# Kernel tuning notes

Hardware: AMD Instinct MI355X
Metric: run time of the kernel (lower is better)

The kernel has to match this reference:

```python
import jax, jax.numpy as jnp
import numpy as np

N_NODES = 100000
LN_EPS = 1e-5
NEG_SLOPE = 0.2


def setup_inputs() -> dict:
    key = jax.random.key(0)
    ks = jax.random.split(key, 6)
    N, E, NIN, EDIM, NOUT, H = N_NODES, 1600000, 64, 32, 128, 4
    x = jax.random.normal(ks[0], (N, NIN), dtype=jnp.float32)
    edge_index = jax.random.randint(ks[1], (2, E), 0, N, dtype=jnp.int64)
    edge_attr = jax.random.normal(ks[2], (E, EDIM), dtype=jnp.float32)
    # xavier-uniform linear weights (torch layout: [out, in])
    def xavier(k, fan_out, fan_in):
        lim = float(np.sqrt(6.0 / (fan_in + fan_out)))
        return jax.random.uniform(k, (fan_out, fan_in), jnp.float32, -lim, lim)
    W_msg = xavier(ks[3], NOUT, NIN + EDIM)          # (128, 96)
    W_att = xavier(ks[4], H, 2 * NIN + EDIM)         # (4, 160)
    bias = jnp.zeros((NOUT,), jnp.float32)
    ln_gamma = jnp.ones((NOUT,), jnp.float32)
    ln_beta = jnp.zeros((NOUT,), jnp.float32)
    return {"x": x, "edge_index": edge_index, "edge_attr": edge_attr,
            "W_msg": W_msg, "W_att": W_att, "bias": bias,
            "ln_gamma": ln_gamma, "ln_beta": ln_beta}


def reference(x, edge_index, edge_attr, W_msg, W_att, bias, ln_gamma, ln_beta):
    N = x.shape[0]
    H = W_att.shape[0]
    src, dst = edge_index[0], edge_index[1]
    xs = x[src]                                       # (E, node_in) gather
    xd = x[dst]                                       # (E, node_in) gather
    # message: W_msg @ [h_u ; x_uv]
    msg_in = jnp.concatenate([xs, edge_attr], axis=-1)            # (E, 96)
    msgs = msg_in @ W_msg.T                                        # (E, out_dim)
    msgs = msgs.reshape(-1, H, W_msg.shape[0] // H)                # (E, H, D)
    # attention logits: LeakyReLU(W_att @ [h_u ; h_v ; x_uv])
    att_in = jnp.concatenate([xs, xd, edge_attr], axis=-1)         # (E, 160)
    logits = att_in @ W_att.T                                      # (E, H)
    logits = jax.nn.leaky_relu(logits, NEG_SLOPE)
    # per-destination-node sparse softmax
    seg_max = jax.ops.segment_max(logits, dst, num_segments=N)     # (N, H)
    exp_l = jnp.exp(logits - seg_max[dst])                         # (E, H)
    seg_sum = jax.ops.segment_sum(exp_l, dst, num_segments=N)      # (N, H)
    att = exp_l / (seg_sum[dst] + 1e-9)                            # (E, H)
    # weighted scatter-add aggregation
    weighted = msgs * att[..., None]                               # (E, H, D)
    out = jax.ops.segment_sum(weighted, dst, num_segments=N)       # (N, H, D)
    out = out.reshape(N, -1) + bias                                # concat heads
    # layer norm over feature dim
    mu = out.mean(axis=-1, keepdims=True)
    var = out.var(axis=-1, keepdims=True)
    out = (out - mu) * jax.lax.rsqrt(var + LN_EPS) * ln_gamma + ln_beta
    return out
```

## Files before the change

### kernel.cpp

```cpp
#include <hip/hip_runtime.h>
#include <hip/hip_bf16.h>

typedef __attribute__((ext_vector_type(8))) short short8;
typedef __attribute__((ext_vector_type(4))) float f32x4;

__device__ __forceinline__ unsigned short fbf(float f) {
  union { float f; unsigned u; } v; v.f = f;
  unsigned r = v.u + 0x7fffu + ((v.u >> 16) & 1u);
  return (unsigned short)(r >> 16);
}
__device__ __forceinline__ unsigned pk2(float a, float b) {
  return (unsigned)fbf(a) | ((unsigned)fbf(b) << 16);
}
__device__ __forceinline__ float ubf(unsigned hi) {
  union { unsigned u; float f; } v; v.u = hi << 16; return v.f;
}
__device__ __forceinline__ float dot4(float4 a, float4 b) {
  return fmaf(a.x, b.x, fmaf(a.y, b.y, fmaf(a.z, b.z, a.w * b.w)));
}

__global__ void k_count(const int* __restrict__ dst, int E, int* __restrict__ deg) {
  for (int i = blockIdx.x * blockDim.x + threadIdx.x; i < E; i += gridDim.x * blockDim.x)
    atomicAdd(&deg[dst[i]], 1);
}

__global__ void k_scan1(const int* __restrict__ deg, int N, int* __restrict__ part,
                        int* __restrict__ bsum) {
  __shared__ int tmp[1024];
  int tid = threadIdx.x;
  int i = blockIdx.x * 1024 + tid;
  int v = (i < N) ? deg[i] : 0;
  tmp[tid] = v;
  __syncthreads();
  for (int ofs = 1; ofs < 1024; ofs <<= 1) {
    int t = (tid >= ofs) ? tmp[tid - ofs] : 0;
    __syncthreads();
    tmp[tid] += t;
    __syncthreads();
  }
  if (i < N) part[i] = tmp[tid] - v;
  if (tid == 1023) bsum[blockIdx.x] = tmp[tid];
}

__global__ void k_scan2(int* __restrict__ part, const int* __restrict__ bsum, int N,
                        int* __restrict__ cursor) {
  __shared__ int sbase;
  if (threadIdx.x == 0) {
    int b = 0;
    for (int j = 0; j < (int)blockIdx.x; j++) b += bsum[j];
    sbase = b;
  }
  __syncthreads();
  int i = blockIdx.x * 1024 + threadIdx.x;
  if (i < N) {
    int o = part[i] + sbase;
    part[i] = o;
    cursor[i] = o;
  }
}

__global__ void k_fill(const int* __restrict__ src, const int* __restrict__ dst, int E,
                       int* __restrict__ cursor, int2* __restrict__ csr2) {
  for (int i = blockIdx.x * blockDim.x + threadIdx.x; i < E; i += gridDim.x * blockDim.x) {
    int d = dst[i];
    int slot = atomicAdd(&cursor[d], 1);
    csr2[slot] = make_int2(src[i], i);
  }
}

__launch_bounds__(256)
__global__ void k_prep(const float* __restrict__ x, const float* __restrict__ W_att,
                       float4* __restrict__ A_s, float4* __restrict__ A_d,
                       unsigned* __restrict__ xb32, int N) {
  __shared__ float4 s_wa[160];
  if (threadIdx.x < 160) s_wa[threadIdx.x] = ((const float4*)W_att)[threadIdx.x];
  __syncthreads();
  for (int v = blockIdx.x * blockDim.x + threadIdx.x; v < N; v += gridDim.x * blockDim.x) {
    const float4* xp = (const float4*)&x[v * 64];
    float4 xq[16];
    #pragma unroll
    for (int k = 0; k < 16; k++) xq[k] = xp[k];
    float as[4] = {}, ad[4] = {};
    #pragma unroll
    for (int h = 0; h < 4; h++) {
      #pragma unroll
      for (int k = 0; k < 16; k++) {
        as[h] += dot4(s_wa[h * 40 + k], xq[k]);
        ad[h] += dot4(s_wa[h * 40 + 16 + k], xq[k]);
      }
    }
    A_s[v] = make_float4(as[0], as[1], as[2], as[3]);
    A_d[v] = make_float4(ad[0], ad[1], ad[2], ad[3]);
    #pragma unroll
    for (int k = 0; k < 16; k++) {
      xb32[v * 32 + 2 * k]     = pk2(xq[k].x, xq[k].y);
      xb32[v * 32 + 2 * k + 1] = pk2(xq[k].z, xq[k].w);
    }
  }
}

__launch_bounds__(256)
__global__ void k_agg(const unsigned short* __restrict__ xb, const float* __restrict__ ea,
                      const float4* __restrict__ A_s, const float4* __restrict__ A_d,
                      const int2* __restrict__ csr2, const int* __restrict__ offsets,
                      const int* __restrict__ deg, const float* __restrict__ W_att,
                      unsigned short* __restrict__ agg, float* __restrict__ denom, int N) {
  __shared__ int2 s_ids[4][32];
  __shared__ float4 s_att[4][8];
  const int lane = threadIdx.x & 63;
  const int wvb = threadIdx.x >> 6;
  const int wv = (blockIdx.x * blockDim.x + threadIdx.x) >> 6;
  const int nw = (gridDim.x * blockDim.x) >> 6;
  const int l32 = lane & 31;
  const bool hi = (lane & 32) != 0;
  const int pj = lane >> 3;
  const int jc = lane & 7;
  const float jc0f = (jc == 0) ? 1.f : 0.f;

  const float4 wea0 = *(const float4*)&W_att[0 * 160 + 128 + jc * 4];
  const float4 wea1 = *(const float4*)&W_att[1 * 160 + 128 + jc * 4];
  const float4 wea2 = *(const float4*)&W_att[2 * 160 + 128 + jc * 4];
  const float4 wea3 = *(const float4*)&W_att[3 * 160 + 128 + jc * 4];

  unsigned short axv[8], bxv[8];
  float aev[8], bev[8];
  float4 aef, aasv, bef, basv;

#define REFILL(g) do {                                                      \
    if (((g) & 3) == 0) {                                                   \
      int2 q_ = csr2[start + min((g) * 8 + l32, dg - 1)];                   \
      if (lane < 32) s_ids[wvb][l32] = q_;                                  \
    }                                                                       \
  } while (0)

#define ISSUE_G(X, E4, AS, g) do {                                          \
    const int qo_ = ((g) & 3) * 8;                                          \
    _Pragma("unroll")                                                       \
    for (int p = 0; p < 8; p++) {                                           \
      int2 t_ = s_ids[wvb][qo_ + p];                                        \
      X[p] = xb[(size_t)t_.x * 64 + lane];                                  \
      E4[p] = ea[(size_t)t_.y * 32 + l32];                                  \
    }                                                                       \
    int2 idl_ = s_ids[wvb][qo_ + pj];                                       \
    AS##ef = *(const float4*)&ea[(size_t)idl_.y * 32 + jc * 4];             \
    AS##asv = A_s[idl_.x];                                                  \
  } while (0)

#define COMPUTE_G(X, E4, AS, g) do {                                        \
    float lp0 = dot4(wea0, AS##ef), lp1 = dot4(wea1, AS##ef);               \
    float lp2 = dot4(wea2, AS##ef), lp3 = dot4(wea3, AS##ef);               \
    _Pragma("unroll")                                                       \
    for (int m = 1; m <= 4; m <<= 1) {                                      \
      lp0 += __shfl_xor(lp0, m, 64); lp1 += __shfl_xor(lp1, m, 64);         \
      lp2 += __shfl_xor(lp2, m, 64); lp3 += __shfl_xor(lp3, m, 64);         \
    }                                                                       \
    const float msk_ = ((g) * 8 + pj < dg) ? 1.f : 0.f;                     \
    float4 av_; float lg_;                                                  \
    lg_ = lp0 + AS##asv.x + adv.x; lg_ = (lg_ > 0.f) ? lg_ : 0.2f * lg_;    \
    av_.x = msk_ * __expf(lg_);                                             \
    lg_ = lp1 + AS##asv.y + adv.y; lg_ = (lg_ > 0.f) ? lg_ : 0.2f * lg_;    \
    av_.y = msk_ * __expf(lg_);                                             \
    lg_ = lp2 + AS##asv.z + adv.z; lg_ = (lg_ > 0.f) ? lg_ : 0.2f * lg_;    \
    av_.z = msk_ * __expf(lg_);                                             \
    lg_ = lp3 + AS##asv.w + adv.w; lg_ = (lg_ > 0.f) ? lg_ : 0.2f * lg_;    \
    av_.w = msk_ * __expf(lg_);                                             \
    if (jc == 0) s_att[wvb][pj] = av_;                                      \
    ssa.x = fmaf(av_.x, jc0f, ssa.x); ssa.y = fmaf(av_.y, jc0f, ssa.y);     \
    ssa.z = fmaf(av_.z, jc0f, ssa.z); ssa.w = fmaf(av_.w, jc0f, ssa.w);     \
    _Pragma("unroll")                                                       \
    for (int p = 0; p < 8; p++) {                                           \
      float4 ap = s_att[wvb][p];                                            \
      float xf = ubf((unsigned)X[p]);                                       \
      ax0 = fmaf(ap.x, xf, ax0); ax1 = fmaf(ap.y, xf, ax1);                 \
      ax2 = fmaf(ap.z, xf, ax2); ax3 = fmaf(ap.w, xf, ax3);                 \
      ae0 = fmaf(hi ? ap.z : ap.x, E4[p], ae0);                             \
      ae1 = fmaf(hi ? ap.w : ap.y, E4[p], ae1);                             \
    }                                                                       \
  } while (0)

  int v = wv;
  int start = 0, dg = 0;
  float4 adv = make_float4(0.f, 0.f, 0.f, 0.f);
  if (v < N) { start = offsets[v]; dg = deg[v]; adv = A_d[v]; }

  while (v < N) {
    const int v_next = v + nw;
    const int vc = min(v_next, N - 1);
    const int start_n = offsets[vc];
    const int dg_n = deg[vc];
    const float4 adv_n = A_d[vc];

    float ax0 = 0, ax1 = 0, ax2 = 0, ax3 = 0, ae0 = 0, ae1 = 0;
    float4 ssa = make_float4(0.f, 0.f, 0.f, 0.f);

    if (dg > 0) {
      const int ng = (dg + 7) >> 3;
      {
        int2 q_ = csr2[start + min(l32, dg - 1)];
        if (lane < 32) s_ids[wvb][l32] = q_;
      }
      ISSUE_G(axv, aev, a, 0);
      int g = 0;
      while (true) {
        if (g + 1 < ng) { REFILL(g + 1); ISSUE_G(bxv, bev, b, g + 1); }
        COMPUTE_G(axv, aev, a, g);
        if (++g >= ng) break;
        if (g + 1 < ng) { REFILL(g + 1); ISSUE_G(axv, aev, a, g + 1); }
        COMPUTE_G(bxv, bev, b, g);
        if (++g >= ng) break;
      }
    }

    #pragma unroll
    for (int m = 1; m <= 32; m <<= 1) {
      ssa.x += __shfl_xor(ssa.x, m, 64);
      ssa.y += __shfl_xor(ssa.y, m, 64);
      ssa.z += __shfl_xor(ssa.z, m, 64);
      ssa.w += __shfl_xor(ssa.w, m, 64);
    }
    const int base = v * 384;
    agg[base + lane]       = fbf(ax0);
    agg[base + 96 + lane]  = fbf(ax1);
    agg[base + 192 + lane] = fbf(ax2);
    agg[base + 288 + lane] = fbf(ax3);
    const int hA = hi ? 2 : 0;
    agg[base + hA * 96 + 64 + l32]       = fbf(ae0);
    agg[base + (hA + 1) * 96 + 64 + l32] = fbf(ae1);
    if (lane == 0) ((float4*)denom)[v] = ssa;

    v = v_next; start = start_n; dg = dg_n; adv = adv_n;
  }
#undef REFILL
#undef ISSUE_G
#undef COMPUTE_G
}

__launch_bounds__(128)
__global__ void k_out(const unsigned short* __restrict__ agg, const float* __restrict__ W_msg,
                      const float* __restrict__ denom, const float* __restrict__ bias,
                      const float* __restrict__ gamma, const float* __restrict__ beta,
                      float* __restrict__ out, int N, int T) {
  __shared__ float s_den[64];
  __shared__ float s_sum[2][16], s_sq[2][16];
  const int f = threadIdx.x;
  const int w = f >> 6;
  const int l = f & 63;
  const int c16 = l & 15;
  const int rg = l >> 4;

  short8 wb[2][2][3];
  float biasv[2][2], gv[2][2], bv[2][2];
  #pragma unroll
  for (int hh = 0; hh < 2; hh++) {
    const int head = 2 * w + hh;
    #pragma unroll
    for (int ct = 0; ct < 2; ct++) {
      const int q = head * 32 + ct * 16 + c16;
      biasv[hh][ct] = bias[q]; gv[hh][ct] = gamma[q]; bv[hh][ct] = beta[q];
      #pragma unroll
      for (int kk = 0; kk < 3; kk++) {
        const float* p = &W_msg[q * 96 + kk * 32 + rg * 8];
        short8 s;
        #pragma unroll
        for (int i = 0; i < 8; i++) s[i] = (short)fbf(p[i]);
        wb[hh][ct][kk] = s;
      }
    }
  }

  for (int t = blockIdx.x; t < T; t += gridDim.x) {
    const int n0 = t * 16;
    if (f < 64) s_den[f] = denom[min(n0 + (f >> 2), N - 1) * 4 + (f & 3)];
    __syncthreads();

    f32x4 c[2][2] = {{{0.f,0.f,0.f,0.f},{0.f,0.f,0.f,0.f}},
                     {{0.f,0.f,0.f,0.f},{0.f,0.f,0.f,0.f}}};
    const int nA = min(n0 + c16, N - 1);
    #pragma unroll
    for (int hh = 0; hh < 2; hh++) {
      const int head = 2 * w + hh;
      #pragma unroll
      for (int kk = 0; kk < 3; kk++) {
        short8 a = *(const short8*)&agg[nA * 384 + head * 96 + kk * 32 + rg * 8];
        c[hh][0] = __builtin_amdgcn_mfma_f32_16x16x32_bf16(a, wb[hh][0][kk], c[hh][0], 0, 0, 0);
        c[hh][1] = __builtin_amdgcn_mfma_f32_16x16x32_bf16(a, wb[hh][1][kk], c[hh][1], 0, 0, 0);
      }
    }

    float val[2][2][4];
    #pragma unroll
    for (int hh = 0; hh < 2; hh++)
      #pragma unroll
      for (int ct = 0; ct < 2; ct++)
        #pragma unroll
        for (int r = 0; r < 4; r++) {
          const float d = s_den[(rg * 4 + r) * 4 + (2 * w + hh)] + 1e-9f;
          val[hh][ct][r] = c[hh][ct][r] / d + biasv[hh][ct];
        }

    float sr[4], qr[4];
    #pragma unroll
    for (int r = 0; r < 4; r++) {
      float s = 0.f, q2 = 0.f;
      #pragma unroll
      for (int hh = 0; hh < 2; hh++)
        #pragma unroll
        for (int ct = 0; ct < 2; ct++) { s += val[hh][ct][r]; q2 = fmaf(val[hh][ct][r], val[hh][ct][r], q2); }
      #pragma unroll
      for (int m = 1; m <= 8; m <<= 1) { s += __shfl_xor(s, m, 64); q2 += __shfl_xor(q2, m, 64); }
      sr[r] = s; qr[r] = q2;
    }
    if (c16 == 0) {
      #pragma unroll
      for (int r = 0; r < 4; r++) { s_sum[w][rg * 4 + r] = sr[r]; s_sq[w][rg * 4 + r] = qr[r]; }
    }
    __syncthreads();

    float mean[4], rstd[4];
    #pragma unroll
    for (int r = 0; r < 4; r++) {
      const int ni = rg * 4 + r;
      mean[r] = (s_sum[0][ni] + s_sum[1][ni]) * (1.f / 128.f);
      const float m2 = (s_sq[0][ni] + s_sq[1][ni]) * (1.f / 128.f);
      rstd[r] = rsqrtf(m2 - mean[r] * mean[r] + 1e-5f);
    }
    #pragma unroll
    for (int hh = 0; hh < 2; hh++)
      #pragma unroll
      for (int ct = 0; ct < 2; ct++)
        #pragma unroll
        for (int r = 0; r < 4; r++) {
          const int n = n0 + rg * 4 + r;
          if (n < N)
            out[n * 128 + (2 * w + hh) * 32 + ct * 16 + c16] =
                (val[hh][ct][r] - mean[r]) * rstd[r] * gv[hh][ct] + bv[hh][ct];
        }
    __syncthreads();
  }
}

extern "C" void kernel_launch(void* const* d_in, const int* in_sizes, int n_in,
                              void* d_out, int out_size, void* d_ws, size_t ws_size,
                              hipStream_t stream) {
  const float* x     = (const float*)d_in[0];
  const int*   ei    = (const int*)d_in[1];
  const float* ea    = (const float*)d_in[2];
  const float* W_msg = (const float*)d_in[3];
  const float* W_att = (const float*)d_in[4];
  const float* bias  = (const float*)d_in[5];
  const float* gamma = (const float*)d_in[6];
  const float* beta  = (const float*)d_in[7];
  float* out = (float*)d_out;

  const int N = in_sizes[0] / 64;
  const int E = in_sizes[1] / 2;
  const int* esrc = ei;
  const int* edst = ei + E;

  char* p = (char*)d_ws;
  int* deg      = (int*)p;            p += (size_t)N * 4;
  int* offsets  = (int*)p;            p += (size_t)N * 4;
  int* cursor   = (int*)p;            p += (size_t)N * 4;
  int* bsum     = (int*)p;            p += 2048 * 4;
  int2* csr2    = (int2*)p;           p += (size_t)E * 8;
  float4* A_s   = (float4*)p;         p += (size_t)N * 16;
  float4* A_d   = (float4*)p;         p += (size_t)N * 16;
  unsigned short* xb = (unsigned short*)p; p += (size_t)N * 64 * 2;
  unsigned short* agg = (unsigned short*)p; p += (size_t)N * 384 * 2;
  float* denom  = (float*)p;

  hipMemsetAsync(deg, 0, (size_t)N * sizeof(int), stream);
  const int SB = (N + 1023) / 1024;
  const int T = (N + 15) / 16;

  k_count<<<2048, 256, 0, stream>>>(edst, E, deg);
  k_scan1<<<SB, 1024, 0, stream>>>(deg, N, offsets, bsum);
  k_scan2<<<SB, 1024, 0, stream>>>(offsets, bsum, N, cursor);
  k_fill<<<2048, 256, 0, stream>>>(esrc, edst, E, cursor, csr2);
  k_prep<<<(N + 255) / 256, 256, 0, stream>>>(x, W_att, A_s, A_d, (unsigned*)xb, N);
  k_agg<<<2048, 256, 0, stream>>>(xb, ea, A_s, A_d, csr2, offsets, deg, W_att,
                                  agg, denom, N);
  k_out<<<2048, 128, 0, stream>>>(agg, W_msg, denom, bias, gamma, beta, out, N, T);
}
```

Measured before the change: 418.7 us.

## Pipeline edge gathers across node boundaries in single-wave aggregation blocks

Restructures the aggregation kernel to one wave per block (8192 blocks of 64 threads) and makes the software pipeline continuous across nodes. The next node's CSR ids are prefetched and the first group of the next node is issued while the current node's last group computes, using double-buffered shared id slots. Edge-attribute loads are halved by having each half-wave load alternate edges and combine through a cross-half shuffle. This is meant to hide gather latency at node boundaries, which is costly with an average degree of about 16, in exchange for more register pressure and more complex control flow.

After: 425.7 us. Within noise of the previous version (+1.7%).

```diff
diff --git a/kernel.cpp b/kernel.cpp
--- a/kernel.cpp
+++ b/kernel.cpp
@@ -99,20 +99,20 @@
   }
 }
 
-__launch_bounds__(256)
+__launch_bounds__(64)
 __global__ void k_agg(const unsigned short* __restrict__ xb, const float* __restrict__ ea,
                       const float4* __restrict__ A_s, const float4* __restrict__ A_d,
                       const int2* __restrict__ csr2, const int* __restrict__ offsets,
                       const int* __restrict__ deg, const float* __restrict__ W_att,
-                      unsigned short* __restrict__ agg, float* __restrict__ denom, int N) {
-  __shared__ int2 s_ids[4][32];
-  __shared__ float4 s_att[4][8];
-  const int lane = threadIdx.x & 63;
-  const int wvb = threadIdx.x >> 6;
-  const int wv = (blockIdx.x * blockDim.x + threadIdx.x) >> 6;
-  const int nw = (gridDim.x * blockDim.x) >> 6;
+                      unsigned short* __restrict__ agg, float* __restrict__ denom,
+                      int N, int Ec) {
+  __shared__ int2 s_ids[2][32];
+  __shared__ float4 s_att[8];
+  const int lane = threadIdx.x;
+  const int nw = gridDim.x;
   const int l32 = lane & 31;
-  const bool hi = (lane & 32) != 0;
+  const bool hi = lane >= 32;
+  const int hsel = hi ? 1 : 0;
   const int pj = lane >> 3;
   const int jc = lane & 7;
   const float jc0f = (jc == 0) ? 1.f : 0.f;
@@ -123,32 +123,28 @@
   const float4 wea3 = *(const float4*)&W_att[3 * 160 + 128 + jc * 4];
 
   unsigned short axv[8], bxv[8];
-  float aev[8], bev[8];
+  float aev[4], bev[4];
   float4 aef, aasv, bef, basv;
 
-#define REFILL(g) do {                                                      \
-    if (((g) & 3) == 0) {                                                   \
-      int2 q_ = csr2[start + min((g) * 8 + l32, dg - 1)];                   \
-      if (lane < 32) s_ids[wvb][l32] = q_;                                  \
-    }                                                                       \
+#define ISSUE_G(X, E4, PF, sl, qo) do {                                     \
+    _Pragma("unroll")                                                       \
+    for (int p = 0; p < 8; p++) {                                           \
+      int2 t_ = s_ids[sl][(qo) + p];                                        \
+      X[p] = xb[(size_t)t_.x * 64 + lane];                                  \
+    }                                                                       \
+    _Pragma("unroll")                                                       \
+    for (int i = 0; i < 4; i++) {                                           \
+      int2 te_ = s_ids[sl][(qo) + 2 * i + hsel];                            \
+      E4[i] = ea[(size_t)te_.y * 32 + l32];                                 \
+    }                                                                       \
+    int2 idl_ = s_ids[sl][(qo) + pj];                                       \
+    PF##ef = *(const float4*)&ea[(size_t)idl_.y * 32 + jc * 4];             \
+    PF##asv = A_s[idl_.x];                                                  \
   } while (0)
 
-#define ISSUE_G(X, E4, AS, g) do {                                          \
-    const int qo_ = ((g) & 3) * 8;                                          \
-    _Pragma("unroll")                                                       \
-    for (int p = 0; p < 8; p++) {                                           \
-      int2 t_ = s_ids[wvb][qo_ + p];                                        \
-      X[p] = xb[(size_t)t_.x * 64 + lane];                                  \
-      E4[p] = ea[(size_t)t_.y * 32 + l32];                                  \
-    }                                                                       \
-    int2 idl_ = s_ids[wvb][qo_ + pj];                                       \
-    AS##ef = *(const float4*)&ea[(size_t)idl_.y * 32 + jc * 4];             \
-    AS##asv = A_s[idl_.x];                                                  \
-  } while (0)
-
-#define COMPUTE_G(X, E4, AS, g) do {                                        \
-    float lp0 = dot4(wea0, AS##ef), lp1 = dot4(wea1, AS##ef);               \
-    float lp2 = dot4(wea2, AS##ef), lp3 = dot4(wea3, AS##ef);               \
+#define COMPUTE_G(X, E4, PF, g) do {                                        \
+    float lp0 = dot4(wea0, PF##ef), lp1 = dot4(wea1, PF##ef);               \
+    float lp2 = dot4(wea2, PF##ef), lp3 = dot4(wea3, PF##ef);               \
     _Pragma("unroll")                                                       \
     for (int m = 1; m <= 4; m <<= 1) {                                      \
       lp0 += __shfl_xor(lp0, m, 64); lp1 += __shfl_xor(lp1, m, 64);         \
@@ -156,83 +152,118 @@
     }                                                                       \
     const float msk_ = ((g) * 8 + pj < dg) ? 1.f : 0.f;                     \
     float4 av_; float lg_;                                                  \
-    lg_ = lp0 + AS##asv.x + adv.x; lg_ = (lg_ > 0.f) ? lg_ : 0.2f * lg_;    \
+    lg_ = lp0 + PF##asv.x + adv.x; lg_ = (lg_ > 0.f) ? lg_ : 0.2f * lg_;    \
     av_.x = msk_ * __expf(lg_);                                             \
-    lg_ = lp1 + AS##asv.y + adv.y; lg_ = (lg_ > 0.f) ? lg_ : 0.2f * lg_;    \
+    lg_ = lp1 + PF##asv.y + adv.y; lg_ = (lg_ > 0.f) ? lg_ : 0.2f * lg_;    \
     av_.y = msk_ * __expf(lg_);                                             \
-    lg_ = lp2 + AS##asv.z + adv.z; lg_ = (lg_ > 0.f) ? lg_ : 0.2f * lg_;    \
+    lg_ = lp2 + PF##asv.z + adv.z; lg_ = (lg_ > 0.f) ? lg_ : 0.2f * lg_;    \
     av_.z = msk_ * __expf(lg_);                                             \
-    lg_ = lp3 + AS##asv.w + adv.w; lg_ = (lg_ > 0.f) ? lg_ : 0.2f * lg_;    \
+    lg_ = lp3 + PF##asv.w + adv.w; lg_ = (lg_ > 0.f) ? lg_ : 0.2f * lg_;    \
     av_.w = msk_ * __expf(lg_);                                             \
-    if (jc == 0) s_att[wvb][pj] = av_;                                      \
+    if (jc == 0) s_att[pj] = av_;                                           \
     ssa.x = fmaf(av_.x, jc0f, ssa.x); ssa.y = fmaf(av_.y, jc0f, ssa.y);     \
     ssa.z = fmaf(av_.z, jc0f, ssa.z); ssa.w = fmaf(av_.w, jc0f, ssa.w);     \
     _Pragma("unroll")                                                       \
     for (int p = 0; p < 8; p++) {                                           \
-      float4 ap = s_att[wvb][p];                                            \
+      float4 ap = s_att[p];                                                 \
       float xf = ubf((unsigned)X[p]);                                       \
       ax0 = fmaf(ap.x, xf, ax0); ax1 = fmaf(ap.y, xf, ax1);                 \
       ax2 = fmaf(ap.z, xf, ax2); ax3 = fmaf(ap.w, xf, ax3);                 \
-      ae0 = fmaf(hi ? ap.z : ap.x, E4[p], ae0);                             \
-      ae1 = fmaf(hi ? ap.w : ap.y, E4[p], ae1);                             \
+    }                                                                       \
+    _Pragma("unroll")                                                       \
+    for (int i = 0; i < 4; i++) {                                           \
+      float4 ap = s_att[2 * i + hsel];                                      \
+      ae0 = fmaf(ap.x, E4[i], ae0); ae1 = fmaf(ap.y, E4[i], ae1);           \
+      ae2 = fmaf(ap.z, E4[i], ae2); ae3 = fmaf(ap.w, E4[i], ae3);           \
     }                                                                       \
   } while (0)
 
-  int v = wv;
-  int start = 0, dg = 0;
-  float4 adv = make_float4(0.f, 0.f, 0.f, 0.f);
-  if (v < N) { start = offsets[v]; dg = deg[v]; adv = A_d[v]; }
-
-  while (v < N) {
-    const int v_next = v + nw;
-    const int vc = min(v_next, N - 1);
-    const int start_n = offsets[vc];
-    const int dg_n = deg[vc];
-    const float4 adv_n = A_d[vc];
-
-    float ax0 = 0, ax1 = 0, ax2 = 0, ax3 = 0, ae0 = 0, ae1 = 0;
-    float4 ssa = make_float4(0.f, 0.f, 0.f, 0.f);
-
-    if (dg > 0) {
-      const int ng = (dg + 7) >> 3;
-      {
-        int2 q_ = csr2[start + min(l32, dg - 1)];
-        if (lane < 32) s_ids[wvb][l32] = q_;
-      }
-      ISSUE_G(axv, aev, a, 0);
-      int g = 0;
-      while (true) {
-        if (g + 1 < ng) { REFILL(g + 1); ISSUE_G(bxv, bev, b, g + 1); }
-        COMPUTE_G(axv, aev, a, g);
-        if (++g >= ng) break;
-        if (g + 1 < ng) { REFILL(g + 1); ISSUE_G(axv, aev, a, g + 1); }
-        COMPUTE_G(bxv, bev, b, g);
-        if (++g >= ng) break;
-      }
-    }
-
-    #pragma unroll
-    for (int m = 1; m <= 32; m <<= 1) {
-      ssa.x += __shfl_xor(ssa.x, m, 64);
-      ssa.y += __shfl_xor(ssa.y, m, 64);
-      ssa.z += __shfl_xor(ssa.z, m, 64);
-      ssa.w += __shfl_xor(ssa.w, m, 64);
-    }
-    const int base = v * 384;
-    agg[base + lane]       = fbf(ax0);
-    agg[base + 96 + lane]  = fbf(ax1);
-    agg[base + 192 + lane] = fbf(ax2);
-    agg[base + 288 + lane] = fbf(ax3);
-    const int hA = hi ? 2 : 0;
-    agg[base + hA * 96 + 64 + l32]       = fbf(ae0);
-    agg[base + (hA + 1) * 96 + 64 + l32] = fbf(ae1);
-    if (lane == 0) ((float4*)denom)[v] = ssa;
-
-    v = v_next; start = start_n; dg = dg_n; adv = adv_n;
-  }
-#undef REFILL
+#define EPILOGUE_G do {                                                     \
+    ae0 += __shfl_xor(ae0, 32, 64); ae1 += __shfl_xor(ae1, 32, 64);         \
+    ae2 += __shfl_xor(ae2, 32, 64); ae3 += __shfl_xor(ae3, 32, 64);         \
+    _Pragma("unroll")                                                       \
+    for (int m = 1; m <= 32; m <<= 1) {                                     \
+      ssa.x += __shfl_xor(ssa.x, m, 64); ssa.y += __shfl_xor(ssa.y, m, 64); \
+      ssa.z += __shfl_xor(ssa.z, m, 64); ssa.w += __shfl_xor(ssa.w, m, 64); \
+    }                                                                       \
+    const int base = v * 384;                                               \
+    agg[base + lane]       = fbf(ax0);                                      \
+    agg[base + 96 + lane]  = fbf(ax1);                                      \
+    agg[base + 192 + lane] = fbf(ax2);                                      \
+    agg[base + 288 + lane] = fbf(ax3);                                      \
+    const int hA = hi ? 2 : 0;                                              \
+    agg[base + hA * 96 + 64 + l32]       = fbf(hi ? ae2 : ae0);             \
+    agg[base + (hA + 1) * 96 + 64 + l32] = fbf(hi ? ae3 : ae1);             \
+    if (lane == 0) ((float4*)denom)[v] = ssa;                               \
+  } while (0)
+
+#define NEXT_NODE do {                                                      \
+    if (vn >= N) { running = false; }                                       \
+    else {                                                                  \
+      v = vn; start = start_n; dg = dg_n; adv = adv_n;                      \
+      ng = (max(dg, 1) + 7) >> 3; g = 0;                                    \
+      vn = v + nw; vc = min(vn, N - 1);                                     \
+      start_n = offsets[vc]; dg_n = deg[vc]; adv_n = A_d[vc];               \
+      qn = csr2[min(start_n + min(l32, max(dg_n, 1) - 1), Ec - 1)];         \
+      ax0 = ax1 = ax2 = ax3 = ae0 = ae1 = ae2 = ae3 = 0.f;                  \
+      ssa = make_float4(0.f, 0.f, 0.f, 0.f);                                \
+    }                                                                       \
+  } while (0)
+
+#define STEP(CX, CE, CP, IX, IE, IP) do {                                   \
+    bool same = (g + 1 < ng);                                               \
+    int nslot = slot, nqo = ((g + 1) & 3) * 8;                              \
+    bool more;                                                              \
+    if (same) {                                                             \
+      if (nqo == 0) {                      \
+        int2 q_ = csr2[min(start + min((g + 1) * 8 + l32, dg - 1), Ec - 1)];\
+        nslot ^= 1; if (!hi) s_ids[nslot][l32] = q_;                        \
+      }                                                                     \
+      more = true;                                                          \
+    } else {                                                                \
+      nslot = slot ^ 1; nqo = 0;                                            \
+      if (!hi) s_ids[nslot][l32] = qn;                                      \
+      more = (vn < N);                                                      \
+    }                                                                       \
+    if (more) ISSUE_G(IX, IE, IP, nslot, nqo);                              \
+    COMPUTE_G(CX, CE, CP, g);                                               \
+    if (!same) { EPILOGUE_G; NEXT_NODE; } else { g++; }                     \
+    slot = nslot;                                                           \
+  } while (0)
+
+  int v = blockIdx.x;
+  if (v >= N) return;
+  int start = offsets[v];
+  int dg = deg[v];
+  float4 adv = A_d[v];
+  int ng = (max(dg, 1) + 7) >> 3;
+  {
+    int2 q_ = csr2[min(start + min(l32, max(dg, 1) - 1), Ec - 1)];
+    if (!hi) s_ids[0][l32] = q_;
+  }
+  int slot = 0;
+  int vn = v + nw, vc = min(vn, N - 1);
+  int start_n = offsets[vc], dg_n = deg[vc];
+  float4 adv_n = A_d[vc];
+  int2 qn = csr2[min(start_n + min(l32, max(dg_n, 1) - 1), Ec - 1)];
+
+  float ax0 = 0, ax1 = 0, ax2 = 0, ax3 = 0;
+  float ae0 = 0, ae1 = 0, ae2 = 0, ae3 = 0;
+  float4 ssa = make_float4(0.f, 0.f, 0.f, 0.f);
+  int g = 0;
+  bool running = true;
+
+  ISSUE_G(axv, aev, a, 0, 0);
+  while (running) {
+    STEP(axv, aev, a, bxv, bev, b);
+    if (!running) break;
+    STEP(bxv, bev, b, axv, aev, a);
+  }
 #undef ISSUE_G
 #undef COMPUTE_G
+#undef EPILOGUE_G
+#undef NEXT_NODE
+#undef STEP
 }
 
 __launch_bounds__(128)
@@ -378,7 +409,7 @@
   k_scan2<<<SB, 1024, 0, stream>>>(offsets, bsum, N, cursor);
   k_fill<<<2048, 256, 0, stream>>>(esrc, edst, E, cursor, csr2);
   k_prep<<<(N + 255) / 256, 256, 0, stream>>>(x, W_att, A_s, A_d, (unsigned*)xb, N);
-  k_agg<<<2048, 256, 0, stream>>>(xb, ea, A_s, A_d, csr2, offsets, deg, W_att,
-                                  agg, denom, N);
+  k_agg<<<8192, 64, 0, stream>>>(xb, ea, A_s, A_d, csr2, offsets, deg, W_att,
+                                 agg, denom, N, E);
   k_out<<<2048, 128, 0, stream>>>(agg, W_msg, denom, bias, gamma, beta, out, N, T);
 }
```
